# Optimization experiments

Hardware: AMD Instinct MI355X
Metric: run time of the kernel (lower is better)

## Reference

```python
import jax, jax.numpy as jnp
import numpy as np
import math

VOCAB = 50000; D = 512; DEPTH = 6; N = 16; DCONV = 4; R = 32; DFF = 4 * D
B = 2; L = 1024

# A = -exp(A_log) with A_log = log(arange(1..N)) repeated over D  =>  A[d,n] = -(n+1)
A_CONT = -jnp.broadcast_to(jnp.arange(1.0, N + 1, dtype=jnp.float32), (D, N))


def sinusoidal(t, dim):
    half = dim // 2
    f = jnp.exp(jnp.arange(half, dtype=jnp.float32) * (-math.log(10000.0) / (half - 1)))
    e = t.astype(jnp.float32)[:, None] * f[None, :]
    return jnp.concatenate([jnp.sin(e), jnp.cos(e)], axis=-1)


def layernorm(x, g, b, eps=1e-5):
    mu = jnp.mean(x, -1, keepdims=True)
    var = jnp.mean((x - mu) ** 2, -1, keepdims=True)
    return (x - mu) * jax.lax.rsqrt(var + eps) * g + b


def ssm(x, Win, Wconv, Wdt, bdt, Dp, Wout):
    # x: [B,L,D]
    proj = x @ Win.T  # [B,L,2D+R+2N]
    xc, z, dtu, Bp, Cp = jnp.split(proj, [D, 2 * D, 2 * D + R, 2 * D + R + N], axis=-1)
    # depthwise causal conv (left pad d_conv-1 == pad both + truncate to L)
    conv = jax.lax.conv_general_dilated(
        xc.transpose(0, 2, 1), Wconv, (1,), [(DCONV - 1, 0)],
        dimension_numbers=('NCH', 'OIH', 'NCH'), feature_group_count=D)
    u = jax.nn.silu(conv.transpose(0, 2, 1))  # [B,L,D]
    dt = jax.nn.softplus(dtu @ Wdt.T + bdt)   # [B,L,D]
    At = jnp.exp(dt[..., None] * A_CONT)      # [B,L,D,N] (ZOH)
    Bu = ((At - 1.0) / (A_CONT + 1e-10)) * Bp[:, :, None, :] * u[..., None]  # [B,L,D,N]

    def step(h, xs):
        a, bu, c = xs
        h = a * h + bu                       # [B,D,N]
        return h, jnp.einsum('bn,bdn->bd', c, h)

    h0 = jnp.zeros((x.shape[0], D, N), dtype=x.dtype)
    _, ys = jax.lax.scan(step, h0, (At.transpose(1, 0, 2, 3), Bu.transpose(1, 0, 2, 3), Cp.transpose(1, 0, 2)))
    y = ys.transpose(1, 0, 2)                # [B,L,D]
    y = (y + u * Dp) * jax.nn.silu(z)
    return y @ Wout.T


def setup_inputs():
    key = jax.random.key(0)
    ks = iter(jax.random.split(key, 32))
    nrm = lambda shape: jax.random.normal(next(ks), shape, jnp.float32) * 0.02
    inp = {
        'x_t': jax.random.randint(next(ks), (B, L), 0, VOCAB + 1),
        't': jax.random.randint(next(ks), (B,), 0, 100),
        'tok_emb': nrm((VOCAB + 1, D)),
        'tmlp_w1': nrm((4 * D, D)), 'tmlp_b1': jnp.zeros((4 * D,)),
        'tmlp_w2': nrm((D, 4 * D)), 'tmlp_b2': jnp.zeros((D,)),
        'ln1_g': jnp.ones((DEPTH, D)), 'ln1_b': jnp.zeros((DEPTH, D)),
        'in_w': nrm((DEPTH, 2 * D + R + 2 * N, D)),
        'conv_w': nrm((DEPTH, D, 1, DCONV)),
        'dt_w': nrm((DEPTH, D, R)), 'dt_b': jnp.zeros((DEPTH, D)),
        'D_p': jnp.ones((DEPTH, D)),
        'out_w': nrm((DEPTH, D, D)),
        'ln2_g': jnp.ones((DEPTH, D)), 'ln2_b': jnp.zeros((DEPTH, D)),
        'mlp_w1': nrm((DEPTH, DFF, D)), 'mlp_b1': jnp.zeros((DEPTH, DFF)),
        'mlp_w2': nrm((DEPTH, D, DFF)), 'mlp_b2': jnp.zeros((DEPTH, D)),
        'lno_g': jnp.ones((D,)), 'lno_b': jnp.zeros((D,)),
        'head_w': nrm((VOCAB, D)), 'head_b': jnp.zeros((VOCAB,)),
    }
    return inp


def reference(x_t, t, tok_emb, tmlp_w1, tmlp_b1, tmlp_w2, tmlp_b2,
              ln1_g, ln1_b, in_w, conv_w, dt_w, dt_b, D_p, out_w,
              ln2_g, ln2_b, mlp_w1, mlp_b1, mlp_w2, mlp_b2,
              lno_g, lno_b, head_w, head_b):
    te = sinusoidal(t, D)
    te = jax.nn.silu(te @ tmlp_w1.T + tmlp_b1) @ tmlp_w2.T + tmlp_b2  # [B,D]
    x = tok_emb[x_t] + te[:, None, :]                                  # [B,L,D]
    for i in range(DEPTH):
        x = x + ssm(layernorm(x, ln1_g[i], ln1_b[i]),
                    in_w[i], conv_w[i], dt_w[i], dt_b[i], D_p[i], out_w[i])
        h = layernorm(x, ln2_g[i], ln2_b[i])
        x = x + jax.nn.gelu(h @ mlp_w1[i].T + mlp_b1[i], approximate=False) @ mlp_w2[i].T + mlp_b2[i]
    x = layernorm(x, lno_g, lno_b)
    return x @ head_w.T + head_b  # [B,L,VOCAB]
```

## Files before the change

kernel.cpp:

```cpp
#include <hip/hip_runtime.h>
#include <hip/hip_bf16.h>
#include <math.h>

typedef __hip_bfloat16 bf16;
typedef short s16x8 __attribute__((ext_vector_type(8)));
typedef float f32x4 __attribute__((ext_vector_type(4)));

#define M_TOK 2048
#define DD    512
#define LSEQ  1024
#define PW    1088
#define NST   16
#define RR    32
#define DFFW  2048
#define NCH   64
#define CH    16
#define PAD   36

__device__ __forceinline__ float bf2f(bf16 v) { return __bfloat162float(v); }
__device__ __forceinline__ float siluf(float x) { return x / (1.f + expf(-x)); }

__device__ __forceinline__ s16x8 cvt8(const f32x4& a, const f32x4& b) {
  s16x8 r;
  r[0] = (short)__bfloat16_as_ushort(__float2bfloat16(a[0]));
  r[1] = (short)__bfloat16_as_ushort(__float2bfloat16(a[1]));
  r[2] = (short)__bfloat16_as_ushort(__float2bfloat16(a[2]));
  r[3] = (short)__bfloat16_as_ushort(__float2bfloat16(a[3]));
  r[4] = (short)__bfloat16_as_ushort(__float2bfloat16(b[0]));
  r[5] = (short)__bfloat16_as_ushort(__float2bfloat16(b[1]));
  r[6] = (short)__bfloat16_as_ushort(__float2bfloat16(b[2]));
  r[7] = (short)__bfloat16_as_ushort(__float2bfloat16(b[3]));
  return r;
}

__constant__ float c_invn[NST] = {
  -1.f/1, -1.f/2, -1.f/3, -1.f/4, -1.f/5, -1.f/6, -1.f/7, -1.f/8,
  -1.f/9, -1.f/10, -1.f/11, -1.f/12, -1.f/13, -1.f/14, -1.f/15, -1.f/16 };

__global__ __launch_bounds__(256) void k_te1(
    const int* __restrict__ t, const float* __restrict__ w1, const float* __restrict__ b1,
    float* __restrict__ h1)
{
  __shared__ float semb[2][512];
  int tid = threadIdx.x;
  float t0 = (float)t[0], t1 = (float)t[1];
  {
    int k = tid;
    float f = expf((float)k * (-9.210340371976184f / 255.f));
    semb[0][k]       = sinf(t0 * f);
    semb[0][k + 256] = cosf(t0 * f);
    semb[1][k]       = sinf(t1 * f);
    semb[1][k + 256] = cosf(t1 * f);
  }
  __syncthreads();
  int wave = tid >> 6, lane = tid & 63;
  int j = blockIdx.x * 4 + wave;
  const float* wr = w1 + (size_t)j * 512;
  float s0 = 0.f, s1 = 0.f;
#pragma unroll
  for (int i = 0; i < 8; ++i) {
    int k = lane + (i << 6);
    float wv = wr[k];
    s0 += wv * semb[0][k];
    s1 += wv * semb[1][k];
  }
  for (int o = 32; o; o >>= 1) { s0 += __shfl_down(s0, o); s1 += __shfl_down(s1, o); }
  if (!lane) {
    float bv = b1[j];
    h1[j]        = siluf(s0 + bv);
    h1[2048 + j] = siluf(s1 + bv);
  }
}

__global__ __launch_bounds__(256) void k_te2(
    const float* __restrict__ h1, const float* __restrict__ w2, const float* __restrict__ b2,
    float* __restrict__ te)
{
  __shared__ float sh1[2][2048];
  int tid = threadIdx.x;
  for (int idx = tid; idx < 4096; idx += 256)
    sh1[idx >> 11][idx & 2047] = h1[idx];
  __syncthreads();
  int wave = tid >> 6, lane = tid & 63;
  int d = blockIdx.x * 4 + wave;
  const float* wr = w2 + (size_t)d * 2048;
  float s0 = 0.f, s1 = 0.f;
#pragma unroll
  for (int i = 0; i < 32; ++i) {
    int k = lane + (i << 6);
    float wv = wr[k];
    s0 += wv * sh1[0][k];
    s1 += wv * sh1[1][k];
  }
  for (int o = 32; o; o >>= 1) { s0 += __shfl_down(s0, o); s1 += __shfl_down(s1, o); }
  if (!lane) {
    float bv = b2[d];
    te[d]       = s0 + bv;
    te[512 + d] = s1 + bv;
  }
}

__global__ __launch_bounds__(256) void k_embed(
    const int* __restrict__ x_t, const float* __restrict__ tok,
    const float* __restrict__ te, float* __restrict__ x)
{
  int m = blockIdx.x;
  int b = m >> 10;
  int row = x_t[m];
  const float* src = tok + (size_t)row * DD;
  for (int d = threadIdx.x; d < DD; d += 256)
    x[(size_t)m * DD + d] = src[d] + te[b * DD + d];
}

__global__ __launch_bounds__(256) void k_layernorm(
    const float* __restrict__ x, const float* __restrict__ g, const float* __restrict__ bb,
    bf16* __restrict__ out)
{
  int m = blockIdx.x;
  const float* xr = x + (size_t)m * DD;
  float2 v = ((const float2*)xr)[threadIdx.x];
  float s = v.x + v.y, ss = v.x * v.x + v.y * v.y;
  for (int o = 32; o; o >>= 1) { s += __shfl_down(s, o); ss += __shfl_down(ss, o); }
  __shared__ float ps[4], pss[4];
  int wave = threadIdx.x >> 6, lane = threadIdx.x & 63;
  if (!lane) { ps[wave] = s; pss[wave] = ss; }
  __syncthreads();
  s = ps[0] + ps[1] + ps[2] + ps[3];
  ss = pss[0] + pss[1] + pss[2] + pss[3];
  float mu = s * (1.f / DD);
  float var = ss * (1.f / DD) - mu * mu;
  float inv = rsqrtf(var + 1e-5f);
  int d = threadIdx.x * 2;
  out[(size_t)m * DD + d]     = __float2bfloat16((v.x - mu) * inv * g[d]     + bb[d]);
  out[(size_t)m * DD + d + 1] = __float2bfloat16((v.y - mu) * inv * g[d + 1] + bb[d + 1]);
}

__global__ __launch_bounds__(256) void k_conv_dt(
    const float* __restrict__ proj, const float* __restrict__ convw,
    const float* __restrict__ dtw, const float* __restrict__ dtb,
    float* __restrict__ u, float* __restrict__ dt)
{
  int m = blockIdx.x >> 1;
  int d = ((blockIdx.x & 1) << 8) + threadIdx.x;
  int b = m >> 10, l = m & 1023;
  __shared__ float dtu[RR];
  if (threadIdx.x < RR) dtu[threadIdx.x] = proj[(size_t)m * PW + 2 * DD + threadIdx.x];
  __syncthreads();
  float c = 0.f;
#pragma unroll
  for (int j = 0; j < 4; ++j) {
    int ll = l - 3 + j;
    if (ll >= 0) c += proj[(size_t)(b * LSEQ + ll) * PW + d] * convw[d * 4 + j];
  }
  u[(size_t)m * DD + d] = siluf(c);
  float s = dtb[d];
  const float* wr = dtw + (size_t)d * RR;
#pragma unroll
  for (int r = 0; r < RR; ++r) s += dtu[r] * wr[r];
  dt[(size_t)m * DD + d] = (s > 0.f) ? (s + log1pf(expf(-s))) : log1pf(expf(s));
}

__global__ __launch_bounds__(128) void k_scan1(
    const float* __restrict__ proj, const float* __restrict__ u,
    const float* __restrict__ dt, float* __restrict__ yloc,
    float* __restrict__ Ebuf, float* __restrict__ Aprod, float* __restrict__ hend)
{
  int d = (blockIdx.x << 7) + threadIdx.x;
  int c = blockIdx.y, b = blockIdx.z;
  int m0 = b * LSEQ + c * CH;
  __shared__ float sBC[CH][32];
  for (int idx = threadIdx.x; idx < CH * 32; idx += 128)
    sBC[idx >> 5][idx & 31] = proj[(size_t)(m0 + (idx >> 5)) * PW + 2 * DD + RR + (idx & 31)];
  __syncthreads();
  float h[NST];
#pragma unroll
  for (int n = 0; n < NST; ++n) h[n] = 0.f;
  float S = 0.f;
  for (int l = 0; l < CH; ++l) {
    size_t m = (size_t)(m0 + l);
    float dtv = dt[m * DD + d];
    float uv  = u[m * DD + d];
    float e1 = expf(-dtv);
    S += dtv;
    Ebuf[m * DD + d] = expf(-S);
    float p = 1.f, acc = 0.f;
#pragma unroll
    for (int n = 0; n < NST; ++n) {
      p *= e1;
      float bu = (p - 1.f) * c_invn[n] * sBC[l][n] * uv;
      h[n] = p * h[n] + bu;
      acc += sBC[l][16 + n] * h[n];
    }
    yloc[m * DD + d] = acc;
  }
  float Ec = expf(-S);
  float p = 1.f;
  size_t base = ((size_t)(b * NCH + c) * NST) * DD + d;
#pragma unroll
  for (int n = 0; n < NST; ++n) {
    p *= Ec;
    Aprod[base + (size_t)n * DD] = p;
    hend [base + (size_t)n * DD] = h[n];
  }
}

__global__ __launch_bounds__(256) void k_scan2(
    const float* __restrict__ Aprod, const float* __restrict__ hend, float* __restrict__ h0)
{
  int idx = blockIdx.x * 256 + threadIdx.x;
  int d = idx & 511;
  int n = (idx >> 9) & 15;
  int b = idx >> 13;
  float h = 0.f;
  for (int c = 0; c < NCH; ++c) {
    size_t o = ((size_t)((b * NCH + c) * NST + n)) * DD + d;
    h0[o] = h;
    h = Aprod[o] * h + hend[o];
  }
}

__global__ __launch_bounds__(128) void k_scan3(
    const float* __restrict__ proj, const float* __restrict__ u,
    const float* __restrict__ yloc, const float* __restrict__ Ebuf,
    const float* __restrict__ h0, const float* __restrict__ Dp, bf16* __restrict__ out)
{
  int d = (blockIdx.x << 7) + threadIdx.x;
  int c = blockIdx.y, b = blockIdx.z;
  int m0 = b * LSEQ + c * CH;
  __shared__ float sC[CH][NST];
  for (int idx = threadIdx.x; idx < CH * NST; idx += 128)
    sC[idx >> 4][idx & 15] = proj[(size_t)(m0 + (idx >> 4)) * PW + 2 * DD + RR + NST + (idx & 15)];
  __syncthreads();
  float hh[NST];
  size_t base = ((size_t)(b * NCH + c) * NST) * DD + d;
#pragma unroll
  for (int n = 0; n < NST; ++n) hh[n] = h0[base + (size_t)n * DD];
  float dpv = Dp[d];
  for (int l = 0; l < CH; ++l) {
    size_t m = (size_t)(m0 + l);
    float E = Ebuf[m * DD + d];
    float p = 1.f, corr = 0.f;
#pragma unroll
    for (int n = 0; n < NST; ++n) {
      p *= E;
      corr += sC[l][n] * p * hh[n];
    }
    float y = yloc[m * DD + d] + corr;
    float z = proj[m * PW + DD + d];
    float v = (y + u[m * DD + d] * dpv) * siluf(z);
    out[m * DD + d] = __float2bfloat16(v);
  }
}

template<int ACT, bool BF16OUT, bool RES, bool BIAS, bool SWZ>
__global__ __launch_bounds__(256) void gemm_abt(
    const bf16* __restrict__ A, const float* __restrict__ B,
    const float* __restrict__ bias, const float* __restrict__ res,
    void* __restrict__ Cout, int N, int K)
{
  __shared__ bf16 sA[128][PAD];
  __shared__ bf16 sB[128][PAD];
  int bn, bm;
  if (SWZ) {
    int flat = blockIdx.y * gridDim.x + blockIdx.x;
    int q = (gridDim.x * gridDim.y) >> 3;
    int s = (flat & 7) * q + (flat >> 3);
    bm = (s % gridDim.x) * 128;
    bn = (s / gridDim.x) * 128;
  } else {
    bn = blockIdx.x * 128;
    bm = blockIdx.y * 128;
  }
  int tid = threadIdx.x;
  int wave = tid >> 6, lane = tid & 63;
  int wm = (wave >> 1) << 6, wn = (wave & 1) << 6;
  int r = lane & 15, q = lane >> 4;
  int ldr = tid >> 2;
  int ldc = (tid & 3) << 3;

  f32x4 acc[4][4];
#pragma unroll
  for (int i = 0; i < 4; ++i)
#pragma unroll
    for (int j = 0; j < 4; ++j) acc[i][j] = (f32x4){0.f, 0.f, 0.f, 0.f};

  s16x8 pa[2];
  f32x4 pb[2][2];
#define GLOAD(k0)                                                              \
  {                                                                            \
    _Pragma("unroll")                                                          \
    for (int h = 0; h < 2; ++h) {                                              \
      int row = ldr + (h << 6);                                                \
      pa[h] = *(const s16x8*)(A + (size_t)(bm + row) * K + (k0) + ldc);        \
      int nrow = bn + row;                                                     \
      if (nrow < N) {                                                          \
        const float* src = B + (size_t)nrow * K + (k0) + ldc;                  \
        pb[h][0] = *(const f32x4*)src;                                         \
        pb[h][1] = *(const f32x4*)(src + 4);                                   \
      } else {                                                                 \
        pb[h][0] = (f32x4){0.f,0.f,0.f,0.f};                                   \
        pb[h][1] = (f32x4){0.f,0.f,0.f,0.f};                                   \
      }                                                                        \
    }                                                                          \
  }

  GLOAD(0);
  for (int k0 = 0; k0 < K; k0 += 32) {
#pragma unroll
    for (int h = 0; h < 2; ++h) {
      int row = ldr + (h << 6);
      *(s16x8*)&sA[row][ldc] = pa[h];
      *(s16x8*)&sB[row][ldc] = cvt8(pb[h][0], pb[h][1]);
    }
    __syncthreads();
    if (k0 + 32 < K) GLOAD(k0 + 32);
    s16x8 af[4], bg[4];
#pragma unroll
    for (int i = 0; i < 4; ++i) af[i] = *(s16x8*)&sA[wm + i * 16 + r][q << 3];
#pragma unroll
    for (int j = 0; j < 4; ++j) bg[j] = *(s16x8*)&sB[wn + j * 16 + r][q << 3];
#pragma unroll
    for (int i = 0; i < 4; ++i)
#pragma unroll
      for (int j = 0; j < 4; ++j)
        acc[i][j] = __builtin_amdgcn_mfma_f32_16x16x32_bf16(af[i], bg[j], acc[i][j], 0, 0, 0);
    __syncthreads();
  }
#undef GLOAD

#pragma unroll
  for (int i = 0; i < 4; ++i)
#pragma unroll
    for (int j = 0; j < 4; ++j) {
      int n = bn + wn + j * 16 + r;
      if (n >= N) continue;
#pragma unroll
      for (int e = 0; e < 4; ++e) {
        int m = bm + wm + i * 16 + (q << 2) + e;
        float v = acc[i][j][e];
        if (BIAS) v += bias[n];
        if (ACT == 1) v = 0.5f * v * (1.f + erff(v * 0.70710678118f));
        if (RES) v += res[(size_t)m * N + n];
        if (BF16OUT) ((bf16*)Cout)[(size_t)m * N + n] = __float2bfloat16(v);
        else         ((float*)Cout)[(size_t)m * N + n] = v;
      }
    }
}

template<int ACT, bool BF16OUT, bool RES, bool BIAS>
__global__ __launch_bounds__(256) void gemm64(
    const bf16* __restrict__ A, const float* __restrict__ B,
    const float* __restrict__ bias, const float* __restrict__ res,
    void* __restrict__ Cout, int N, int K)
{
  __shared__ bf16 sA[64][PAD];
  __shared__ bf16 sB[64][PAD];
  int bn = blockIdx.x * 64;
  int bm = blockIdx.y * 64;
  int tid = threadIdx.x;
  int wave = tid >> 6, lane = tid & 63;
  int wm = (wave >> 1) << 5, wn = (wave & 1) << 5;
  int r = lane & 15, q = lane >> 4;
  int ldr = tid >> 2;
  int ldc = (tid & 3) << 3;

  f32x4 acc[2][2];
#pragma unroll
  for (int i = 0; i < 2; ++i)
#pragma unroll
    for (int j = 0; j < 2; ++j) acc[i][j] = (f32x4){0.f, 0.f, 0.f, 0.f};

  s16x8 pa;
  f32x4 pb[2];
#define GLOAD64(k0)                                                            \
  {                                                                            \
    pa = *(const s16x8*)(A + (size_t)(bm + ldr) * K + (k0) + ldc);             \
    const float* src = B + (size_t)(bn + ldr) * K + (k0) + ldc;                \
    pb[0] = *(const f32x4*)src;                                                \
    pb[1] = *(const f32x4*)(src + 4);                                          \
  }

  GLOAD64(0);
  for (int k0 = 0; k0 < K; k0 += 32) {
    *(s16x8*)&sA[ldr][ldc] = pa;
    *(s16x8*)&sB[ldr][ldc] = cvt8(pb[0], pb[1]);
    __syncthreads();
    if (k0 + 32 < K) GLOAD64(k0 + 32);
    s16x8 af[2], bg[2];
#pragma unroll
    for (int i = 0; i < 2; ++i) af[i] = *(s16x8*)&sA[wm + i * 16 + r][q << 3];
#pragma unroll
    for (int j = 0; j < 2; ++j) bg[j] = *(s16x8*)&sB[wn + j * 16 + r][q << 3];
#pragma unroll
    for (int i = 0; i < 2; ++i)
#pragma unroll
      for (int j = 0; j < 2; ++j)
        acc[i][j] = __builtin_amdgcn_mfma_f32_16x16x32_bf16(af[i], bg[j], acc[i][j], 0, 0, 0);
    __syncthreads();
  }
#undef GLOAD64

#pragma unroll
  for (int i = 0; i < 2; ++i)
#pragma unroll
    for (int j = 0; j < 2; ++j) {
      int n = bn + wn + j * 16 + r;
#pragma unroll
      for (int e = 0; e < 4; ++e) {
        int m = bm + wm + i * 16 + (q << 2) + e;
        float v = acc[i][j][e];
        if (BIAS) v += bias[n];
        if (ACT == 1) v = 0.5f * v * (1.f + erff(v * 0.70710678118f));
        if (RES) v += res[(size_t)m * N + n];
        if (BF16OUT) ((bf16*)Cout)[(size_t)m * N + n] = __float2bfloat16(v);
        else         ((float*)Cout)[(size_t)m * N + n] = v;
      }
    }
}

extern "C" void kernel_launch(void* const* d_in, const int* in_sizes, int n_in,
                              void* d_out, int out_size, void* d_ws, size_t ws_size,
                              hipStream_t stream) {
  const int*   x_t     = (const int*)d_in[0];
  const int*   t       = (const int*)d_in[1];
  const float* tok_emb = (const float*)d_in[2];
  const float* tmlp_w1 = (const float*)d_in[3];
  const float* tmlp_b1 = (const float*)d_in[4];
  const float* tmlp_w2 = (const float*)d_in[5];
  const float* tmlp_b2 = (const float*)d_in[6];
  const float* ln1_g   = (const float*)d_in[7];
  const float* ln1_b   = (const float*)d_in[8];
  const float* in_w    = (const float*)d_in[9];
  const float* conv_w  = (const float*)d_in[10];
  const float* dt_w    = (const float*)d_in[11];
  const float* dt_b    = (const float*)d_in[12];
  const float* D_p     = (const float*)d_in[13];
  const float* out_w   = (const float*)d_in[14];
  const float* ln2_g   = (const float*)d_in[15];
  const float* ln2_b   = (const float*)d_in[16];
  const float* mlp_w1  = (const float*)d_in[17];
  const float* mlp_b1  = (const float*)d_in[18];
  const float* mlp_w2  = (const float*)d_in[19];
  const float* mlp_b2  = (const float*)d_in[20];
  const float* lno_g   = (const float*)d_in[21];
  const float* lno_b   = (const float*)d_in[22];
  const float* head_w  = (const float*)d_in[23];
  const float* head_b  = (const float*)d_in[24];

  char* w = (char*)d_ws;
  float* te    = (float*)w;  w += 4096;
  float* h1t   = (float*)w;  w += 16384;
  float* x     = (float*)w;  w += (size_t)M_TOK * DD * 4;
  bf16*  aIn   = (bf16*)w;   w += (size_t)M_TOK * DD * 2;
  float* proj  = (float*)w;  w += (size_t)M_TOK * PW * 4;
  float* ubuf  = (float*)w;  w += (size_t)M_TOK * DD * 4;
  float* dtbuf = (float*)w;  w += (size_t)M_TOK * DD * 4;
  float* ybuf  = (float*)w;  w += (size_t)M_TOK * DD * 4;
  float* Ebuf  = (float*)w;  w += (size_t)M_TOK * DD * 4;
  float* Aprod = (float*)w;  w += (size_t)2 * NCH * NST * DD * 4;
  float* hend  = (float*)w;  w += (size_t)2 * NCH * NST * DD * 4;
  float* h0    = (float*)w;  w += (size_t)2 * NCH * NST * DD * 4;
  bf16*  gbuf  = (bf16*)proj;

  k_te1<<<512, 256, 0, stream>>>(t, tmlp_w1, tmlp_b1, h1t);
  k_te2<<<128, 256, 0, stream>>>(h1t, tmlp_w2, tmlp_b2, te);
  k_embed<<<M_TOK, 256, 0, stream>>>(x_t, tok_emb, te, x);

  for (int i = 0; i < 6; ++i) {
    const float* inw_i  = in_w   + (size_t)i * PW * DD;
    const float* cw_i   = conv_w + (size_t)i * DD * 4;
    const float* dtw_i  = dt_w   + (size_t)i * DD * RR;
    const float* dtb_i  = dt_b   + (size_t)i * DD;
    const float* dp_i   = D_p    + (size_t)i * DD;
    const float* ow_i   = out_w  + (size_t)i * DD * DD;
    const float* m1_i   = mlp_w1 + (size_t)i * DFFW * DD;
    const float* m1b_i  = mlp_b1 + (size_t)i * DFFW;
    const float* m2_i   = mlp_w2 + (size_t)i * DD * DFFW;
    const float* m2b_i  = mlp_b2 + (size_t)i * DD;

    k_layernorm<<<M_TOK, 256, 0, stream>>>(x, ln1_g + i * DD, ln1_b + i * DD, aIn);
    gemm64<0,false,false,false><<<dim3(PW / 64, M_TOK / 64), 256, 0, stream>>>(
        aIn, inw_i, nullptr, nullptr, proj, PW, DD);
    k_conv_dt<<<M_TOK * 2, 256, 0, stream>>>(proj, cw_i, dtw_i, dtb_i, ubuf, dtbuf);
    k_scan1<<<dim3(4, NCH, 2), 128, 0, stream>>>(proj, ubuf, dtbuf, ybuf, Ebuf, Aprod, hend);
    k_scan2<<<2 * NST * DD / 256, 256, 0, stream>>>(Aprod, hend, h0);
    k_scan3<<<dim3(4, NCH, 2), 128, 0, stream>>>(proj, ubuf, ybuf, Ebuf, h0, dp_i, aIn);
    gemm64<0,false,true,false><<<dim3(DD / 64, M_TOK / 64), 256, 0, stream>>>(
        aIn, ow_i, nullptr, x, x, DD, DD);
    k_layernorm<<<M_TOK, 256, 0, stream>>>(x, ln2_g + i * DD, ln2_b + i * DD, aIn);
    gemm64<1,true,false,true><<<dim3(DFFW / 64, M_TOK / 64), 256, 0, stream>>>(
        aIn, m1_i, m1b_i, nullptr, gbuf, DFFW, DD);
    gemm64<0,false,true,true><<<dim3(DD / 64, M_TOK / 64), 256, 0, stream>>>(
        gbuf, m2_i, m2b_i, x, x, DD, DFFW);
  }

  k_layernorm<<<M_TOK, 256, 0, stream>>>(x, lno_g, lno_b, aIn);
  gemm_abt<0,false,false,true,true><<<dim3(M_TOK / 128, (50000 + 127) / 128), 256, 0, stream>>>(
      aIn, head_w, head_b, nullptr, d_out, 50000, DD);
}
```

Baseline: 1.222 ms.

## Pre-convert weights to bf16 and use direct global-to-LDS load GEMMs

Adds a conversion kernel that turns the fp32 weights (in_w, out_w, mlp, head) into bf16 copies in the workspace on every call, padding the head weights to a multiple of 128 rows. New GEMM kernels then load both operands straight into LDS with global_load_lds, instead of loading fp32 weights into registers, converting them and storing them to LDS inside each GEMM. This removes repeated per-tile conversion and halves the weight bytes the GEMMs read. In exchange it adds extra memory traffic for the conversion pass, and the new loop has no register prefetch, so load latency is less hidden. The new path only runs when the workspace is large enough.

```diff
diff --git a/kernel.cpp b/kernel.cpp
--- a/kernel.cpp
+++ b/kernel.cpp
@@ -16,6 +16,8 @@
 #define NCH   64
 #define CH    16
 #define PAD   36
+#define NHEAD 50000
+#define NHEADP 50048
 
 __device__ __forceinline__ float bf2f(bf16 v) { return __bfloat162float(v); }
 __device__ __forceinline__ float siluf(float x) { return x / (1.f + expf(-x)); }
@@ -33,9 +35,29 @@
   return r;
 }
 
+__device__ __forceinline__ void gload16(const bf16* g, bf16* l) {
+  __builtin_amdgcn_global_load_lds((const __attribute__((address_space(1))) void*)g,
+                                   (__attribute__((address_space(3))) void*)l, 16, 0, 0);
+}
+
 __constant__ float c_invn[NST] = {
   -1.f/1, -1.f/2, -1.f/3, -1.f/4, -1.f/5, -1.f/6, -1.f/7, -1.f/8,
   -1.f/9, -1.f/10, -1.f/11, -1.f/12, -1.f/13, -1.f/14, -1.f/15, -1.f/16 };
+
+__global__ __launch_bounds__(256) void k_cvt(
+    const float* __restrict__ src, bf16* __restrict__ dst, int n_src, int n_dst)
+{
+  for (int i = (blockIdx.x * 256 + threadIdx.x) * 8; i < n_dst; i += gridDim.x * 256 * 8) {
+    s16x8 v;
+    if (i + 8 <= n_src) {
+      f32x4 a = *(const f32x4*)(src + i), b = *(const f32x4*)(src + i + 4);
+      v = cvt8(a, b);
+    } else {
+      v = (s16x8){0,0,0,0,0,0,0,0};
+    }
+    *(s16x8*)((short*)dst + i) = v;
+  }
+}
 
 __global__ __launch_bounds__(256) void k_te1(
     const int* __restrict__ t, const float* __restrict__ w1, const float* __restrict__ b1,
@@ -252,6 +274,141 @@
   }
 }
 
+template<int ACT, bool BF16OUT, bool RES, bool BIAS>
+__global__ __launch_bounds__(256) void gemm_bb128(
+    const bf16* __restrict__ A, const bf16* __restrict__ B,
+    const float* __restrict__ bias, const float* __restrict__ res,
+    void* __restrict__ Cout, int N, int K)
+{
+  __shared__ bf16 sA[128 * 32];
+  __shared__ bf16 sB[128 * 32];
+  int flat = blockIdx.y * gridDim.x + blockIdx.x;
+  int qq = (gridDim.x * gridDim.y) >> 3;
+  int s = (flat & 7) * qq + (flat >> 3);
+  int bm = (s % gridDim.x) * 128;
+  int bn = (s / gridDim.x) * 128;
+  int tid = threadIdx.x;
+  int wave = tid >> 6, lane = tid & 63;
+  int wm = (wave >> 1) << 6, wn = (wave & 1) << 6;
+  int r = lane & 15, q = lane >> 4;
+  int srow = (wave << 4) + (lane >> 2);
+  int scol = (lane & 3) << 3;
+  const bf16* pA = A + (size_t)(bm + srow) * K + scol;
+  const bf16* pB = B + (size_t)(bn + srow) * K + scol;
+  bf16* lA = sA + ((wave << 4) << 5);
+  bf16* lB = sB + ((wave << 4) << 5);
+
+  f32x4 acc[4][4];
+#pragma unroll
+  for (int i = 0; i < 4; ++i)
+#pragma unroll
+    for (int j = 0; j < 4; ++j) acc[i][j] = (f32x4){0.f, 0.f, 0.f, 0.f};
+
+  for (int k0 = 0; k0 < K; k0 += 32) {
+    gload16(pA,                  lA);
+    gload16(pA + (size_t)64 * K, lA + 64 * 32);
+    gload16(pB,                  lB);
+    gload16(pB + (size_t)64 * K, lB + 64 * 32);
+    pA += 32; pB += 32;
+    __syncthreads();
+    s16x8 af[4], bg[4];
+#pragma unroll
+    for (int i = 0; i < 4; ++i) af[i] = *(s16x8*)&sA[((wm + i * 16 + r) << 5) + (q << 3)];
+#pragma unroll
+    for (int j = 0; j < 4; ++j) bg[j] = *(s16x8*)&sB[((wn + j * 16 + r) << 5) + (q << 3)];
+#pragma unroll
+    for (int i = 0; i < 4; ++i)
+#pragma unroll
+      for (int j = 0; j < 4; ++j)
+        acc[i][j] = __builtin_amdgcn_mfma_f32_16x16x32_bf16(af[i], bg[j], acc[i][j], 0, 0, 0);
+    __syncthreads();
+  }
+
+#pragma unroll
+  for (int i = 0; i < 4; ++i)
+#pragma unroll
+    for (int j = 0; j < 4; ++j) {
+      int n = bn + wn + j * 16 + r;
+      if (n >= N) continue;
+#pragma unroll
+      for (int e = 0; e < 4; ++e) {
+        int m = bm + wm + i * 16 + (q << 2) + e;
+        float v = acc[i][j][e];
+        if (BIAS) v += bias[n];
+        if (ACT == 1) v = 0.5f * v * (1.f + erff(v * 0.70710678118f));
+        if (RES) v += res[(size_t)m * N + n];
+        if (BF16OUT) ((bf16*)Cout)[(size_t)m * N + n] = __float2bfloat16(v);
+        else         ((float*)Cout)[(size_t)m * N + n] = v;
+      }
+    }
+}
+
+template<int ACT, bool BF16OUT, bool RES, bool BIAS>
+__global__ __launch_bounds__(256) void gemm_bb64(
+    const bf16* __restrict__ A, const bf16* __restrict__ B,
+    const float* __restrict__ bias, const float* __restrict__ res,
+    void* __restrict__ Cout, int N, int K)
+{
+  __shared__ bf16 sA[64 * 32];
+  __shared__ bf16 sB[64 * 32];
+  int flat = blockIdx.y * gridDim.x + blockIdx.x;
+  int qq = (gridDim.x * gridDim.y) >> 3;
+  int s = (flat & 7) * qq + (flat >> 3);
+  int bm = (s % gridDim.x) * 64;
+  int bn = (s / gridDim.x) * 64;
+  int tid = threadIdx.x;
+  int wave = tid >> 6, lane = tid & 63;
+  int wm = (wave >> 1) << 5, wn = (wave & 1) << 5;
+  int r = lane & 15, q = lane >> 4;
+  int srow = (wave << 4) + (lane >> 2);
+  int scol = (lane & 3) << 3;
+  const bf16* pA = A + (size_t)(bm + srow) * K + scol;
+  const bf16* pB = B + (size_t)(bn + srow) * K + scol;
+  bf16* lA = sA + ((wave << 4) << 5);
+  bf16* lB = sB + ((wave << 4) << 5);
+
+  f32x4 acc[2][2];
+#pragma unroll
+  for (int i = 0; i < 2; ++i)
+#pragma unroll
+    for (int j = 0; j < 2; ++j) acc[i][j] = (f32x4){0.f, 0.f, 0.f, 0.f};
+
+  for (int k0 = 0; k0 < K; k0 += 32) {
+    gload16(pA, lA);
+    gload16(pB, lB);
+    pA += 32; pB += 32;
+    __syncthreads();
+    s16x8 af[2], bg[2];
+#pragma unroll
+    for (int i = 0; i < 2; ++i) af[i] = *(s16x8*)&sA[((wm + i * 16 + r) << 5) + (q << 3)];
+#pragma unroll
+    for (int j = 0; j < 2; ++j) bg[j] = *(s16x8*)&sB[((wn + j * 16 + r) << 5) + (q << 3)];
+#pragma unroll
+    for (int i = 0; i < 2; ++i)
+#pragma unroll
+      for (int j = 0; j < 2; ++j)
+        acc[i][j] = __builtin_amdgcn_mfma_f32_16x16x32_bf16(af[i], bg[j], acc[i][j], 0, 0, 0);
+    __syncthreads();
+  }
+
+#pragma unroll
+  for (int i = 0; i < 2; ++i)
+#pragma unroll
+    for (int j = 0; j < 2; ++j) {
+      int n = bn + wn + j * 16 + r;
+#pragma unroll
+      for (int e = 0; e < 4; ++e) {
+        int m = bm + wm + i * 16 + (q << 2) + e;
+        float v = acc[i][j][e];
+        if (BIAS) v += bias[n];
+        if (ACT == 1) v = 0.5f * v * (1.f + erff(v * 0.70710678118f));
+        if (RES) v += res[(size_t)m * N + n];
+        if (BF16OUT) ((bf16*)Cout)[(size_t)m * N + n] = __float2bfloat16(v);
+        else         ((float*)Cout)[(size_t)m * N + n] = v;
+      }
+    }
+}
+
 template<int ACT, bool BF16OUT, bool RES, bool BIAS, bool SWZ>
 __global__ __launch_bounds__(256) void gemm_abt(
     const bf16* __restrict__ A, const float* __restrict__ B,
@@ -277,13 +434,11 @@
   int r = lane & 15, q = lane >> 4;
   int ldr = tid >> 2;
   int ldc = (tid & 3) << 3;
-
   f32x4 acc[4][4];
 #pragma unroll
   for (int i = 0; i < 4; ++i)
 #pragma unroll
     for (int j = 0; j < 4; ++j) acc[i][j] = (f32x4){0.f, 0.f, 0.f, 0.f};
-
   s16x8 pa[2];
   f32x4 pb[2][2];
 #define GLOAD(k0)                                                              \
@@ -303,7 +458,6 @@
       }                                                                        \
     }                                                                          \
   }
-
   GLOAD(0);
   for (int k0 = 0; k0 < K; k0 += 32) {
 #pragma unroll
@@ -327,7 +481,6 @@
     __syncthreads();
   }
 #undef GLOAD
-
 #pragma unroll
   for (int i = 0; i < 4; ++i)
 #pragma unroll
@@ -363,13 +516,11 @@
   int r = lane & 15, q = lane >> 4;
   int ldr = tid >> 2;
   int ldc = (tid & 3) << 3;
-
   f32x4 acc[2][2];
 #pragma unroll
   for (int i = 0; i < 2; ++i)
 #pragma unroll
     for (int j = 0; j < 2; ++j) acc[i][j] = (f32x4){0.f, 0.f, 0.f, 0.f};
-
   s16x8 pa;
   f32x4 pb[2];
 #define GLOAD64(k0)                                                            \
@@ -379,7 +530,6 @@
     pb[0] = *(const f32x4*)src;                                                \
     pb[1] = *(const f32x4*)(src + 4);                                          \
   }
-
   GLOAD64(0);
   for (int k0 = 0; k0 < K; k0 += 32) {
     *(s16x8*)&sA[ldr][ldc] = pa;
@@ -399,7 +549,6 @@
     __syncthreads();
   }
 #undef GLOAD64
-
 #pragma unroll
   for (int i = 0; i < 2; ++i)
 #pragma unroll
@@ -461,40 +610,68 @@
   float* hend  = (float*)w;  w += (size_t)2 * NCH * NST * DD * 4;
   float* h0    = (float*)w;  w += (size_t)2 * NCH * NST * DD * 4;
   bf16*  gbuf  = (bf16*)proj;
+  bf16* bw_in   = (bf16*)w;  w += (size_t)6 * PW * DD * 2;
+  bf16* bw_out  = (bf16*)w;  w += (size_t)6 * DD * DD * 2;
+  bf16* bw_m1   = (bf16*)w;  w += (size_t)6 * DFFW * DD * 2;
+  bf16* bw_m2   = (bf16*)w;  w += (size_t)6 * DD * DFFW * 2;
+  bf16* bw_head = (bf16*)w;  w += (size_t)NHEADP * DD * 2;
+  bool fast = ((size_t)(w - (char*)d_ws) <= ws_size);
+
+  if (fast) {
+    k_cvt<<<1024, 256, 0, stream>>>(in_w,   bw_in,   6 * PW * DD,   6 * PW * DD);
+    k_cvt<<<1024, 256, 0, stream>>>(out_w,  bw_out,  6 * DD * DD,   6 * DD * DD);
+    k_cvt<<<1024, 256, 0, stream>>>(mlp_w1, bw_m1,   6 * DFFW * DD, 6 * DFFW * DD);
+    k_cvt<<<1024, 256, 0, stream>>>(mlp_w2, bw_m2,   6 * DD * DFFW, 6 * DD * DFFW);
+    k_cvt<<<2048, 256, 0, stream>>>(head_w, bw_head, NHEAD * DD,    NHEADP * DD);
+  }
 
   k_te1<<<512, 256, 0, stream>>>(t, tmlp_w1, tmlp_b1, h1t);
   k_te2<<<128, 256, 0, stream>>>(h1t, tmlp_w2, tmlp_b2, te);
   k_embed<<<M_TOK, 256, 0, stream>>>(x_t, tok_emb, te, x);
 
   for (int i = 0; i < 6; ++i) {
-    const float* inw_i  = in_w   + (size_t)i * PW * DD;
     const float* cw_i   = conv_w + (size_t)i * DD * 4;
     const float* dtw_i  = dt_w   + (size_t)i * DD * RR;
     const float* dtb_i  = dt_b   + (size_t)i * DD;
     const float* dp_i   = D_p    + (size_t)i * DD;
-    const float* ow_i   = out_w  + (size_t)i * DD * DD;
-    const float* m1_i   = mlp_w1 + (size_t)i * DFFW * DD;
     const float* m1b_i  = mlp_b1 + (size_t)i * DFFW;
-    const float* m2_i   = mlp_w2 + (size_t)i * DD * DFFW;
     const float* m2b_i  = mlp_b2 + (size_t)i * DD;
 
     k_layernorm<<<M_TOK, 256, 0, stream>>>(x, ln1_g + i * DD, ln1_b + i * DD, aIn);
-    gemm64<0,false,false,false><<<dim3(PW / 64, M_TOK / 64), 256, 0, stream>>>(
-        aIn, inw_i, nullptr, nullptr, proj, PW, DD);
+    if (fast)
+      gemm_bb64<0,false,false,false><<<dim3(M_TOK / 64, PW / 64), 256, 0, stream>>>(
+          aIn, bw_in + (size_t)i * PW * DD, nullptr, nullptr, proj, PW, DD);
+    else
+      gemm64<0,false,false,false><<<dim3(PW / 64, M_TOK / 64), 256, 0, stream>>>(
+          aIn, in_w + (size_t)i * PW * DD, nullptr, nullptr, proj, PW, DD);
     k_conv_dt<<<M_TOK * 2, 256, 0, stream>>>(proj, cw_i, dtw_i, dtb_i, ubuf, dtbuf);
     k_scan1<<<dim3(4, NCH, 2), 128, 0, stream>>>(proj, ubuf, dtbuf, ybuf, Ebuf, Aprod, hend);
     k_scan2<<<2 * NST * DD / 256, 256, 0, stream>>>(Aprod, hend, h0);
     k_scan3<<<dim3(4, NCH, 2), 128, 0, stream>>>(proj, ubuf, ybuf, Ebuf, h0, dp_i, aIn);
-    gemm64<0,false,true,false><<<dim3(DD / 64, M_TOK / 64), 256, 0, stream>>>(
-        aIn, ow_i, nullptr, x, x, DD, DD);
-    k_layernorm<<<M_TOK, 256, 0, stream>>>(x, ln2_g + i * DD, ln2_b + i * DD, aIn);
-    gemm64<1,true,false,true><<<dim3(DFFW / 64, M_TOK / 64), 256, 0, stream>>>(
-        aIn, m1_i, m1b_i, nullptr, gbuf, DFFW, DD);
-    gemm64<0,false,true,true><<<dim3(DD / 64, M_TOK / 64), 256, 0, stream>>>(
-        gbuf, m2_i, m2b_i, x, x, DD, DFFW);
+    if (fast) {
+      gemm_bb64<0,false,true,false><<<dim3(M_TOK / 64, DD / 64), 256, 0, stream>>>(
+          aIn, bw_out + (size_t)i * DD * DD, nullptr, x, x, DD, DD);
+      k_layernorm<<<M_TOK, 256, 0, stream>>>(x, ln2_g + i * DD, ln2_b + i * DD, aIn);
+      gemm_bb128<1,true,false,true><<<dim3(M_TOK / 128, DFFW / 128), 256, 0, stream>>>(
+          aIn, bw_m1 + (size_t)i * DFFW * DD, m1b_i, nullptr, gbuf, DFFW, DD);
+      gemm_bb64<0,false,true,true><<<dim3(M_TOK / 64, DD / 64), 256, 0, stream>>>(
+          gbuf, bw_m2 + (size_t)i * DD * DFFW, m2b_i, x, x, DD, DFFW);
+    } else {
+      gemm64<0,false,true,false><<<dim3(DD / 64, M_TOK / 64), 256, 0, stream>>>(
+          aIn, out_w + (size_t)i * DD * DD, nullptr, x, x, DD, DD);
+      k_layernorm<<<M_TOK, 256, 0, stream>>>(x, ln2_g + i * DD, ln2_b + i * DD, aIn);
+      gemm64<1,true,false,true><<<dim3(DFFW / 64, M_TOK / 64), 256, 0, stream>>>(
+          aIn, mlp_w1 + (size_t)i * DFFW * DD, m1b_i, nullptr, gbuf, DFFW, DD);
+      gemm64<0,false,true,true><<<dim3(DD / 64, M_TOK / 64), 256, 0, stream>>>(
+          gbuf, mlp_w2 + (size_t)i * DD * DFFW, m2b_i, x, x, DD, DFFW);
+    }
   }
 
   k_layernorm<<<M_TOK, 256, 0, stream>>>(x, lno_g, lno_b, aIn);
-  gemm_abt<0,false,false,true,true><<<dim3(M_TOK / 128, (50000 + 127) / 128), 256, 0, stream>>>(
-      aIn, head_w, head_b, nullptr, d_out, 50000, DD);
-}
+  if (fast)
+    gemm_bb128<0,false,false,true><<<dim3(M_TOK / 128, NHEADP / 128), 256, 0, stream>>>(
+        aIn, bw_head, head_b, nullptr, d_out, NHEAD, DD);
+  else
+    gemm_abt<0,false,false,true,true><<<dim3(M_TOK / 128, (NHEAD + 127) / 128), 256, 0, stream>>>(
+        aIn, head_w, head_b, nullptr, d_out, NHEAD, DD);
+}
```

Result: faster. 1.160 ms (-5.1%).
